# Optimization experiments

Measured on AMD Instinct MI355X. Metric: run time of the kernel, lower is better.

## Reference

```python
import jax, jax.numpy as jnp
import numpy as np

EPS = 1e-6
L, H, D, DFF = 4, 6, 6, 64  # n_layers, num_heads(=dim, head_dim=1), d_hid, ffn hidden


def layernorm(x, w, b):
    mu = jnp.mean(x, axis=-1, keepdims=True)
    var = jnp.mean((x - mu) ** 2, axis=-1, keepdims=True)
    return (x - mu) / jnp.sqrt(var + EPS) * w + b


def autocorr(x, qw, qb, kw, kb, vw, vb, l1w, l1b):
    # x: [B,S,H]; head_dim==1 so per-head Linear is scalar w*x+b per head.
    k_in = jnp.concatenate([x[:, :1], x[:, :-1]], axis=1)   # roll right, first row kept
    v_in = jnp.concatenate([x[:, 1:], x[:, -1:]], axis=1)   # roll left, last row kept
    q = x * qw + qb
    k = k_in * kw + kb
    v = v_in * vw + vb
    teo = q * q - k * v                                      # [B,S,H]
    # nn.LayerNorm([1]) over size-1 axis: mean==x, var==0 -> output is bias
    normed = (teo - teo) / jnp.sqrt(EPS) * l1w + l1b
    scores = jax.nn.softmax(normed, axis=1)                  # over seq dim
    return scores * teo


def mha(x, p, li, ai):
    out = autocorr(x, p['qw'][li, ai], p['qb'][li, ai], p['kw'][li, ai],
                   p['kb'][li, ai], p['vw'][li, ai], p['vb'][li, ai],
                   p['ln1_w'][li, ai], p['ln1_b'][li, ai])
    return layernorm(out + x, p['mha_ln_w'][li, ai], p['mha_ln_b'][li, ai])


def setup_inputs() -> dict:
    key = jax.random.key(0)
    ks = jax.random.split(key, 24)
    n = jax.random.normal
    inp = {
        'x_batch': n(ks[0], (128, 4096, 6), jnp.float32),
        'enc_output': n(ks[1], (128, 4096, 6), jnp.float32),
        'dec_ln_w': jnp.ones((D,), jnp.float32),
        'dec_ln_b': jnp.zeros((D,), jnp.float32),
        'qw': n(ks[2], (L, 2, H), jnp.float32),
        'qb': n(ks[3], (L, 2, H), jnp.float32) * 0.1,
        'kw': n(ks[4], (L, 2, H), jnp.float32),
        'kb': n(ks[5], (L, 2, H), jnp.float32) * 0.1,
        'vw': n(ks[6], (L, 2, H), jnp.float32),
        'vb': n(ks[7], (L, 2, H), jnp.float32) * 0.1,
        'ln1_w': jnp.ones((L, 2), jnp.float32),
        'ln1_b': jnp.zeros((L, 2), jnp.float32),
        'mha_ln_w': jnp.ones((L, 2, D), jnp.float32),
        'mha_ln_b': jnp.zeros((L, 2, D), jnp.float32),
        'ffn_w1': n(ks[8], (L, DFF, D), jnp.float32) * (1.0 / np.sqrt(D)),
        'ffn_b1': jnp.zeros((L, DFF), jnp.float32),
        'ffn_w2': n(ks[9], (L, D, DFF), jnp.float32) * (1.0 / np.sqrt(DFF)),
        'ffn_b2': jnp.zeros((L, D), jnp.float32),
        'ffn_ln_w': jnp.ones((L, D), jnp.float32),
        'ffn_ln_b': jnp.zeros((L, D), jnp.float32),
    }
    return inp


def reference(x_batch, enc_output, dec_ln_w, dec_ln_b, qw, qb, kw, kb, vw, vb,
              ln1_w, ln1_b, mha_ln_w, mha_ln_b, ffn_w1, ffn_b1, ffn_w2, ffn_b2,
              ffn_ln_w, ffn_ln_b):
    p = dict(qw=qw, qb=qb, kw=kw, kb=kb, vw=vw, vb=vb, ln1_w=ln1_w, ln1_b=ln1_b,
             mha_ln_w=mha_ln_w, mha_ln_b=mha_ln_b)
    x = layernorm(x_batch, dec_ln_w, dec_ln_b)  # dropout p=0 -> identity
    for li in range(L):
        x = mha(x, p, li, 0)   # self-attention block
        x = mha(x, p, li, 1)   # "enc" attention block (also self, per source)
        h = jax.nn.relu(jnp.einsum('bsd,fd->bsf', x, ffn_w1[li]) + ffn_b1[li])
        y = jnp.einsum('bsf,df->bsd', h, ffn_w2[li]) + ffn_b2[li] + x
        x = layernorm(y, ffn_ln_w[li], ffn_ln_b[li])
    return x
```

## Files before the change

kernel.cpp:

```cpp
#include <hip/hip_runtime.h>

#define S_LEN  4096
#define DM     6
#define NLAYER 4
#define NFF    64
#define HALO   8
#define TPB    256
#define OUT_PER_WAVE 112
#define BLK_X 10

typedef float    vf2 __attribute__((ext_vector_type(2)));
typedef float    vf4 __attribute__((ext_vector_type(4)));
typedef _Float16 vh4 __attribute__((ext_vector_type(4)));

#define XSZ (128*16)
#define YSTRIDE 130
#define YSZ (6*YSTRIDE*4)
#define WAVE_LDS (XSZ + YSZ)

__device__ __forceinline__ vf2 splat2(float s){ vf2 r; r.x = s; r.y = s; return r; }
__device__ __forceinline__ unsigned pkh(float a, float b){
    return __builtin_bit_cast(unsigned, __builtin_amdgcn_cvt_pkrtz(a, b));
}

__device__ __forceinline__ void ln6v(vf2* v, const float* __restrict__ w,
                                     const float* __restrict__ b) {
    vf2 mu = (((v[0]+v[1])+(v[2]+v[3]))+(v[4]+v[5])) * (1.0f/6.0f);
    vf2 var = splat2(0.0f);
#pragma unroll
    for (int d = 0; d < DM; ++d) { vf2 dd = v[d]-mu; var = __builtin_elementwise_fma(dd, dd, var); }
    vf2 a = var * (1.0f/6.0f) + splat2(1e-6f);
    vf2 r; r.x = rsqrtf(a.x); r.y = rsqrtf(a.y);
#pragma unroll
    for (int d = 0; d < DM; ++d)
        v[d] = __builtin_elementwise_fma((v[d]-mu)*r, splat2(w[d]), splat2(b[d]));
}

__global__ __launch_bounds__(TPB)
void decoder_fused(const float* __restrict__ x_batch,
                   const float* __restrict__ dec_ln_w, const float* __restrict__ dec_ln_b,
                   const float* __restrict__ qw, const float* __restrict__ qb,
                   const float* __restrict__ kw, const float* __restrict__ kb,
                   const float* __restrict__ vw, const float* __restrict__ vb,
                   const float* __restrict__ mha_ln_w, const float* __restrict__ mha_ln_b,
                   const float* __restrict__ ffn_w1, const float* __restrict__ ffn_b1,
                   const float* __restrict__ ffn_w2, const float* __restrict__ ffn_b2,
                   const float* __restrict__ ffn_ln_w, const float* __restrict__ ffn_ln_b,
                   float* __restrict__ out) {
    const int lane = threadIdx.x & 63;
    const int wid  = threadIdx.x >> 6;
    const int w    = blockIdx.x * (TPB/64) + wid;
    const int b    = blockIdx.y;
    const int p    = w * OUT_PER_WAVE - HALO + 2*lane;
    const int c    = lane & 15, g = lane >> 4;

    __shared__ __align__(16) char smem[(TPB/64) * WAVE_LDS];
    char* wbase = smem + wid * WAVE_LDS;
    char* Xb = wbase;
    char* Yb = wbase + XSZ;

    vf2 x2[DM];
    if (p >= 0 && p + 1 < S_LEN) {
        const float4* s = reinterpret_cast<const float4*>(x_batch + ((size_t)b*S_LEN + p)*DM);
        float4 a0 = s[0], a1 = s[1], a2 = s[2];
        x2[0].x=a0.x; x2[1].x=a0.y; x2[2].x=a0.z; x2[3].x=a0.w; x2[4].x=a1.x; x2[5].x=a1.y;
        x2[0].y=a1.z; x2[1].y=a1.w; x2[2].y=a2.x; x2[3].y=a2.y; x2[4].y=a2.z; x2[5].y=a2.w;
    } else {
        const int pc = min(max(p, 0), S_LEN-1);
        const float2* s = reinterpret_cast<const float2*>(x_batch + ((size_t)b*S_LEN + pc)*DM);
        float2 a0 = s[0], a1 = s[1], a2 = s[2];
        x2[0] = splat2(a0.x); x2[1] = splat2(a0.y); x2[2] = splat2(a1.x);
        x2[3] = splat2(a1.y); x2[4] = splat2(a2.x); x2[5] = splat2(a2.y);
    }

    ln6v(x2, dec_ln_w, dec_ln_b);

#pragma unroll 1
    for (int li = 0; li < NLAYER; ++li) {
        vh4 w1f[4], w2f[4]; vf4 b1f[4];
#pragma unroll
        for (int mt = 0; mt < 4; ++mt) {
            const int f = mt*16 + c;
            float4 a = make_float4(0.f, 0.f, 0.f, 0.f);
            if (g == 0) {
                float2 u = *reinterpret_cast<const float2*>(ffn_w1 + li*NFF*DM + f*DM);
                float2 v = *reinterpret_cast<const float2*>(ffn_w1 + li*NFF*DM + f*DM + 2);
                a = make_float4(u.x, u.y, v.x, v.y);
            } else if (g == 1) {
                float2 u = *reinterpret_cast<const float2*>(ffn_w1 + li*NFF*DM + f*DM + 4);
                a = make_float4(u.x, u.y, 0.f, 0.f);
            }
            uint2 ua = make_uint2(pkh(a.x, a.y), pkh(a.z, a.w));
            w1f[mt] = __builtin_bit_cast(vh4, ua);

            float4 wv = make_float4(0.f, 0.f, 0.f, 0.f);
            if (c < DM)
                wv = *reinterpret_cast<const float4*>(ffn_w2 + li*DM*NFF + c*NFF + mt*16 + g*4);
            uint2 uw = make_uint2(pkh(wv.x, wv.y), pkh(wv.z, wv.w));
            w2f[mt] = __builtin_bit_cast(vh4, uw);

            float4 bb = *reinterpret_cast<const float4*>(ffn_b1 + li*NFF + mt*16 + g*4);
            vf4 bv; bv.x=bb.x; bv.y=bb.y; bv.z=bb.z; bv.w=bb.w;
            b1f[mt] = bv;
        }

#pragma unroll 1
        for (int ai = 0; ai < 2; ++ai) {
            const int base = (li*2 + ai) * DM;
            vf2 xm[DM], xp[DM];
#pragma unroll
            for (int d = 0; d < DM; ++d) {
                float up = __shfl_up (x2[d].y, 1);
                float dn = __shfl_down(x2[d].x, 1);
                xm[d].x = (p <= 0) ? x2[d].x : up;
                xm[d].y = x2[d].x;
                xp[d].x = x2[d].y;
                xp[d].y = (p + 1 >= S_LEN - 1) ? x2[d].y : dn;
            }
#pragma unroll
            for (int d = 0; d < DM; ++d) {
                vf2 q = __builtin_elementwise_fma(x2[d], splat2(qw[base+d]), splat2(qb[base+d]));
                vf2 k = __builtin_elementwise_fma(xm[d], splat2(kw[base+d]), splat2(kb[base+d]));
                vf2 v = __builtin_elementwise_fma(xp[d], splat2(vw[base+d]), splat2(vb[base+d]));
                vf2 teo = __builtin_elementwise_fma(q, q, -(k*v));
                x2[d] = __builtin_elementwise_fma(teo, splat2(1.0f/(float)S_LEN), x2[d]);
            }
            ln6v(x2, mha_ln_w + base, mha_ln_b + base);
        }

        {
            {
                char* r0 = Xb + lane*32;
                *(uint4*)r0      = make_uint4(pkh(x2[0].x,x2[1].x), pkh(x2[2].x,x2[3].x),
                                              pkh(x2[4].x,x2[5].x), 0u);
                *(uint4*)(r0+16) = make_uint4(pkh(x2[0].y,x2[1].y), pkh(x2[2].y,x2[3].y),
                                              pkh(x2[4].y,x2[5].y), 0u);
            }
            vh4 bfrag[8];
#pragma unroll
            for (int t = 0; t < 8; ++t) {
                vh4 v = *(const vh4*)(Xb + (16*t + c)*16 + (g&1)*8);
                if (g >= 2) v = (vh4)(_Float16)0;
                bfrag[t] = v;
            }

#pragma unroll
            for (int t = 0; t < 8; ++t) {
                vh4 hb[4];
#pragma unroll
                for (int ft = 0; ft < 4; ++ft) {
                    vf4 hc = __builtin_amdgcn_mfma_f32_16x16x16f16(w1f[ft], bfrag[t], b1f[ft], 0, 0, 0);
                    uint2 u = make_uint2(pkh(hc.x,hc.y), pkh(hc.z,hc.w));
                    vh4 hraw = __builtin_bit_cast(vh4, u);
                    vh4 z4 = (vh4)(_Float16)0;
                    hb[ft] = __builtin_elementwise_max(hraw, z4);
                }
                vf4 yacc; yacc.x=0.f; yacc.y=0.f; yacc.z=0.f; yacc.w=0.f;
#pragma unroll
                for (int ks = 0; ks < 4; ++ks)
                    yacc = __builtin_amdgcn_mfma_f32_16x16x16f16(w2f[ks], hb[ks], yacc, 0, 0, 0);
                int col = 16*t + c;
                float* yp = (float*)Yb;
                if (lane < 32) {
                    yp[(g*4+0)*YSTRIDE + col] = yacc.x;
                    yp[(g*4+1)*YSTRIDE + col] = yacc.y;
                }
                if (lane < 16) {
                    yp[2*YSTRIDE + col] = yacc.z;
                    yp[3*YSTRIDE + col] = yacc.w;
                }
            }
            const float* b2 = ffn_b2 + li*DM;
#pragma unroll
            for (int d = 0; d < DM; ++d) {
                float2 yv = *(const float2*)((float*)Yb + d*YSTRIDE + 2*lane);
                vf2 t2; t2.x = yv.x; t2.y = yv.y;
                x2[d] = x2[d] + splat2(b2[d]) + t2;
            }
            ln6v(x2, ffn_ln_w + li*DM, ffn_ln_b + li*DM);
        }
    }

    if (lane >= 4 && lane < 60 && p < S_LEN) {
        float4* dst = reinterpret_cast<float4*>(out + ((size_t)b*S_LEN + p)*DM);
        float4 a0, a1, a2;
        a0.x=x2[0].x; a0.y=x2[1].x; a0.z=x2[2].x; a0.w=x2[3].x;
        a1.x=x2[4].x; a1.y=x2[5].x; a1.z=x2[0].y; a1.w=x2[1].y;
        a2.x=x2[2].y; a2.y=x2[3].y; a2.z=x2[4].y; a2.w=x2[5].y;
        dst[0]=a0; dst[1]=a1; dst[2]=a2;
    }
}

extern "C" void kernel_launch(void* const* d_in, const int* in_sizes, int n_in,
                              void* d_out, int out_size, void* d_ws, size_t ws_size,
                              hipStream_t stream) {
    const float* x_batch  = (const float*)d_in[0];
    const float* dec_ln_w = (const float*)d_in[2];
    const float* dec_ln_b = (const float*)d_in[3];
    const float* qw       = (const float*)d_in[4];
    const float* qb       = (const float*)d_in[5];
    const float* kw       = (const float*)d_in[6];
    const float* kb       = (const float*)d_in[7];
    const float* vw       = (const float*)d_in[8];
    const float* vb       = (const float*)d_in[9];
    const float* mha_ln_w = (const float*)d_in[12];
    const float* mha_ln_b = (const float*)d_in[13];
    const float* ffn_w1   = (const float*)d_in[14];
    const float* ffn_b1   = (const float*)d_in[15];
    const float* ffn_w2   = (const float*)d_in[16];
    const float* ffn_b2   = (const float*)d_in[17];
    const float* ffn_ln_w = (const float*)d_in[18];
    const float* ffn_ln_b = (const float*)d_in[19];
    float* out = (float*)d_out;

    const int B = in_sizes[0] / (S_LEN * DM);
    dim3 grid(BLK_X, B);
    decoder_fused<<<grid, TPB, 0, stream>>>(
        x_batch, dec_ln_w, dec_ln_b, qw, qb, kw, kb, vw, vb,
        mha_ln_w, mha_ln_b, ffn_w1, ffn_b1, ffn_w2, ffn_b2,
        ffn_ln_w, ffn_ln_b, out);
}
```

Baseline: 140.8 us.

## Process four positions per lane with single-wave blocks and fp16 halo/Y exchange

```diff
diff --git a/kernel.cpp b/kernel.cpp
--- a/kernel.cpp
+++ b/kernel.cpp
@@ -5,35 +5,37 @@
 #define NLAYER 4
 #define NFF    64
 #define HALO   8
-#define TPB    256
-#define OUT_PER_WAVE 112
-#define BLK_X 10
-
-typedef float    vf2 __attribute__((ext_vector_type(2)));
+#define TPB    64
+#define PPL    4
+#define OUT_PER_WAVE 240
+#define WBX    18
+
 typedef float    vf4 __attribute__((ext_vector_type(4)));
+typedef _Float16 vh2 __attribute__((ext_vector_type(2)));
 typedef _Float16 vh4 __attribute__((ext_vector_type(4)));
 
-#define XSZ (128*16)
-#define YSTRIDE 130
-#define YSZ (6*YSTRIDE*4)
-#define WAVE_LDS (XSZ + YSZ)
-
-__device__ __forceinline__ vf2 splat2(float s){ vf2 r; r.x = s; r.y = s; return r; }
+#define XSZ      (256*16)
+#define YSTRIDE  260
+#define YSZ      (3*YSTRIDE*4)
+#define LDS_TOT  (XSZ + YSZ)
+
+__device__ __forceinline__ vf4 splat4(float s){ vf4 r; r.x=s;r.y=s;r.z=s;r.w=s; return r; }
 __device__ __forceinline__ unsigned pkh(float a, float b){
     return __builtin_bit_cast(unsigned, __builtin_amdgcn_cvt_pkrtz(a, b));
 }
-
-__device__ __forceinline__ void ln6v(vf2* v, const float* __restrict__ w,
-                                     const float* __restrict__ b) {
-    vf2 mu = (((v[0]+v[1])+(v[2]+v[3]))+(v[4]+v[5])) * (1.0f/6.0f);
-    vf2 var = splat2(0.0f);
-#pragma unroll
-    for (int d = 0; d < DM; ++d) { vf2 dd = v[d]-mu; var = __builtin_elementwise_fma(dd, dd, var); }
-    vf2 a = var * (1.0f/6.0f) + splat2(1e-6f);
-    vf2 r; r.x = rsqrtf(a.x); r.y = rsqrtf(a.y);
+__device__ __forceinline__ vh2 bch2(unsigned u){ return __builtin_bit_cast(vh2, u); }
+
+__device__ __forceinline__ void ln6v4(vf4* v, const float* __restrict__ w,
+                                      const float* __restrict__ b) {
+    vf4 mu = (((v[0]+v[1])+(v[2]+v[3]))+(v[4]+v[5])) * (1.0f/6.0f);
+    vf4 var = splat4(0.0f);
+#pragma unroll
+    for (int d = 0; d < DM; ++d) { vf4 dd = v[d]-mu; var = __builtin_elementwise_fma(dd, dd, var); }
+    vf4 a = var * (1.0f/6.0f) + splat4(1e-6f);
+    vf4 r; r.x=rsqrtf(a.x); r.y=rsqrtf(a.y); r.z=rsqrtf(a.z); r.w=rsqrtf(a.w);
 #pragma unroll
     for (int d = 0; d < DM; ++d)
-        v[d] = __builtin_elementwise_fma((v[d]-mu)*r, splat2(w[d]), splat2(b[d]));
+        v[d] = __builtin_elementwise_fma((v[d]-mu)*r, splat4(w[d]), splat4(b[d]));
 }
 
 __global__ __launch_bounds__(TPB)
@@ -47,33 +49,42 @@
                    const float* __restrict__ ffn_w2, const float* __restrict__ ffn_b2,
                    const float* __restrict__ ffn_ln_w, const float* __restrict__ ffn_ln_b,
                    float* __restrict__ out) {
-    const int lane = threadIdx.x & 63;
-    const int wid  = threadIdx.x >> 6;
-    const int w    = blockIdx.x * (TPB/64) + wid;
+    const int lane = threadIdx.x;
+    const int w    = blockIdx.x;
     const int b    = blockIdx.y;
-    const int p    = w * OUT_PER_WAVE - HALO + 2*lane;
+    const int p0   = w * OUT_PER_WAVE - HALO + PPL*lane;
     const int c    = lane & 15, g = lane >> 4;
 
-    __shared__ __align__(16) char smem[(TPB/64) * WAVE_LDS];
-    char* wbase = smem + wid * WAVE_LDS;
-    char* Xb = wbase;
-    char* Yb = wbase + XSZ;
-
-    vf2 x2[DM];
-    if (p >= 0 && p + 1 < S_LEN) {
-        const float4* s = reinterpret_cast<const float4*>(x_batch + ((size_t)b*S_LEN + p)*DM);
-        float4 a0 = s[0], a1 = s[1], a2 = s[2];
-        x2[0].x=a0.x; x2[1].x=a0.y; x2[2].x=a0.z; x2[3].x=a0.w; x2[4].x=a1.x; x2[5].x=a1.y;
-        x2[0].y=a1.z; x2[1].y=a1.w; x2[2].y=a2.x; x2[3].y=a2.y; x2[4].y=a2.z; x2[5].y=a2.w;
+    __shared__ __align__(16) char smem[LDS_TOT];
+    char* Xb = smem;
+    char* Yb = smem + XSZ;
+
+    vf4 x4[DM];
+    if (p0 >= 0 && p0 + PPL <= S_LEN) {
+        const float4* s = reinterpret_cast<const float4*>(x_batch + ((size_t)b*S_LEN + p0)*DM);
+        float4 a0=s[0],a1=s[1],a2=s[2],a3=s[3],a4=s[4],a5=s[5];
+        x4[0] = (vf4){a0.x, a1.z, a3.x, a4.z};
+        x4[1] = (vf4){a0.y, a1.w, a3.y, a4.w};
+        x4[2] = (vf4){a0.z, a2.x, a3.z, a5.x};
+        x4[3] = (vf4){a0.w, a2.y, a3.w, a5.y};
+        x4[4] = (vf4){a1.x, a2.z, a4.x, a5.z};
+        x4[5] = (vf4){a1.y, a2.w, a4.y, a5.w};
     } else {
-        const int pc = min(max(p, 0), S_LEN-1);
-        const float2* s = reinterpret_cast<const float2*>(x_batch + ((size_t)b*S_LEN + pc)*DM);
-        float2 a0 = s[0], a1 = s[1], a2 = s[2];
-        x2[0] = splat2(a0.x); x2[1] = splat2(a0.y); x2[2] = splat2(a1.x);
-        x2[3] = splat2(a1.y); x2[4] = splat2(a2.x); x2[5] = splat2(a2.y);
+        float tmp[PPL][DM];
+#pragma unroll
+        for (int s = 0; s < PPL; ++s) {
+            const int pc = min(max(p0 + s, 0), S_LEN-1);
+            const float2* f2 = reinterpret_cast<const float2*>(x_batch + ((size_t)b*S_LEN + pc)*DM);
+            float2 u0 = f2[0], u1 = f2[1], u2 = f2[2];
+            tmp[s][0]=u0.x; tmp[s][1]=u0.y; tmp[s][2]=u1.x;
+            tmp[s][3]=u1.y; tmp[s][4]=u2.x; tmp[s][5]=u2.y;
+        }
+#pragma unroll
+        for (int d = 0; d < DM; ++d)
+            x4[d] = (vf4){tmp[0][d], tmp[1][d], tmp[2][d], tmp[3][d]};
     }
 
-    ln6v(x2, dec_ln_w, dec_ln_b);
+    ln6v4(x4, dec_ln_w, dec_ln_b);
 
 #pragma unroll 1
     for (int li = 0; li < NLAYER; ++li) {
@@ -100,94 +111,99 @@
             w2f[mt] = __builtin_bit_cast(vh4, uw);
 
             float4 bb = *reinterpret_cast<const float4*>(ffn_b1 + li*NFF + mt*16 + g*4);
-            vf4 bv; bv.x=bb.x; bv.y=bb.y; bv.z=bb.z; bv.w=bb.w;
-            b1f[mt] = bv;
+            b1f[mt] = (vf4){bb.x, bb.y, bb.z, bb.w};
         }
 
 #pragma unroll 1
         for (int ai = 0; ai < 2; ++ai) {
             const int base = (li*2 + ai) * DM;
-            vf2 xm[DM], xp[DM];
+            unsigned s3a = pkh(x4[0].w, x4[1].w), s3b = pkh(x4[2].w, x4[3].w), s3c = pkh(x4[4].w, x4[5].w);
+            unsigned s0a = pkh(x4[0].x, x4[1].x), s0b = pkh(x4[2].x, x4[3].x), s0c = pkh(x4[4].x, x4[5].x);
+            unsigned ua = __shfl_up((int)s3a, 1), ub = __shfl_up((int)s3b, 1), uc = __shfl_up((int)s3c, 1);
+            unsigned da = __shfl_down((int)s0a, 1), db = __shfl_down((int)s0b, 1), dc = __shfl_down((int)s0c, 1);
+            float pm[DM], pp[DM];
+            { vh2 h; h=bch2(ua); pm[0]=(float)h.x; pm[1]=(float)h.y;
+                     h=bch2(ub); pm[2]=(float)h.x; pm[3]=(float)h.y;
+                     h=bch2(uc); pm[4]=(float)h.x; pm[5]=(float)h.y;
+                     h=bch2(da); pp[0]=(float)h.x; pp[1]=(float)h.y;
+                     h=bch2(db); pp[2]=(float)h.x; pp[3]=(float)h.y;
+                     h=bch2(dc); pp[4]=(float)h.x; pp[5]=(float)h.y; }
+            const bool first = (p0 <= 0);
+            const bool last  = (p0 + PPL - 1 >= S_LEN - 1);
 #pragma unroll
             for (int d = 0; d < DM; ++d) {
-                float up = __shfl_up (x2[d].y, 1);
-                float dn = __shfl_down(x2[d].x, 1);
-                xm[d].x = (p <= 0) ? x2[d].x : up;
-                xm[d].y = x2[d].x;
-                xp[d].x = x2[d].y;
-                xp[d].y = (p + 1 >= S_LEN - 1) ? x2[d].y : dn;
-            }
-#pragma unroll
-            for (int d = 0; d < DM; ++d) {
-                vf2 q = __builtin_elementwise_fma(x2[d], splat2(qw[base+d]), splat2(qb[base+d]));
-                vf2 k = __builtin_elementwise_fma(xm[d], splat2(kw[base+d]), splat2(kb[base+d]));
-                vf2 v = __builtin_elementwise_fma(xp[d], splat2(vw[base+d]), splat2(vb[base+d]));
-                vf2 teo = __builtin_elementwise_fma(q, q, -(k*v));
-                x2[d] = __builtin_elementwise_fma(teo, splat2(1.0f/(float)S_LEN), x2[d]);
-            }
-            ln6v(x2, mha_ln_w + base, mha_ln_b + base);
+                float prevv = first ? x4[d].x : pm[d];
+                float nextv = last  ? x4[d].w : pp[d];
+                vf4 xm = (vf4){prevv,   x4[d].x, x4[d].y, x4[d].z};
+                vf4 xp = (vf4){x4[d].y, x4[d].z, x4[d].w, nextv};
+                vf4 q = __builtin_elementwise_fma(x4[d], splat4(qw[base+d]), splat4(qb[base+d]));
+                vf4 k = __builtin_elementwise_fma(xm,    splat4(kw[base+d]), splat4(kb[base+d]));
+                vf4 v = __builtin_elementwise_fma(xp,    splat4(vw[base+d]), splat4(vb[base+d]));
+                vf4 teo = __builtin_elementwise_fma(q, q, -(k*v));
+                x4[d] = __builtin_elementwise_fma(teo, splat4(1.0f/(float)S_LEN), x4[d]);
+            }
+            ln6v4(x4, mha_ln_w + base, mha_ln_b + base);
         }
 
         {
             {
-                char* r0 = Xb + lane*32;
-                *(uint4*)r0      = make_uint4(pkh(x2[0].x,x2[1].x), pkh(x2[2].x,x2[3].x),
-                                              pkh(x2[4].x,x2[5].x), 0u);
-                *(uint4*)(r0+16) = make_uint4(pkh(x2[0].y,x2[1].y), pkh(x2[2].y,x2[3].y),
-                                              pkh(x2[4].y,x2[5].y), 0u);
-            }
-            vh4 bfrag[8];
-#pragma unroll
-            for (int t = 0; t < 8; ++t) {
+                char* r0 = Xb + lane*64;
+                *(uint4*)(r0)    = make_uint4(pkh(x4[0].x,x4[1].x), pkh(x4[2].x,x4[3].x), pkh(x4[4].x,x4[5].x), 0u);
+                *(uint4*)(r0+16) = make_uint4(pkh(x4[0].y,x4[1].y), pkh(x4[2].y,x4[3].y), pkh(x4[4].y,x4[5].y), 0u);
+                *(uint4*)(r0+32) = make_uint4(pkh(x4[0].z,x4[1].z), pkh(x4[2].z,x4[3].z), pkh(x4[4].z,x4[5].z), 0u);
+                *(uint4*)(r0+48) = make_uint4(pkh(x4[0].w,x4[1].w), pkh(x4[2].w,x4[3].w), pkh(x4[4].w,x4[5].w), 0u);
+            }
+            vh4 bfrag[16];
+#pragma unroll
+            for (int t = 0; t < 16; ++t) {
                 vh4 v = *(const vh4*)(Xb + (16*t + c)*16 + (g&1)*8);
                 if (g >= 2) v = (vh4)(_Float16)0;
                 bfrag[t] = v;
             }
 
 #pragma unroll
-            for (int t = 0; t < 8; ++t) {
+            for (int t = 0; t < 16; ++t) {
                 vh4 hb[4];
 #pragma unroll
                 for (int ft = 0; ft < 4; ++ft) {
                     vf4 hc = __builtin_amdgcn_mfma_f32_16x16x16f16(w1f[ft], bfrag[t], b1f[ft], 0, 0, 0);
                     uint2 u = make_uint2(pkh(hc.x,hc.y), pkh(hc.z,hc.w));
                     vh4 hraw = __builtin_bit_cast(vh4, u);
-                    vh4 z4 = (vh4)(_Float16)0;
-                    hb[ft] = __builtin_elementwise_max(hraw, z4);
+                    hb[ft] = __builtin_elementwise_max(hraw, (vh4)(_Float16)0);
                 }
                 vf4 yacc; yacc.x=0.f; yacc.y=0.f; yacc.z=0.f; yacc.w=0.f;
 #pragma unroll
                 for (int ks = 0; ks < 4; ++ks)
                     yacc = __builtin_amdgcn_mfma_f32_16x16x16f16(w2f[ks], hb[ks], yacc, 0, 0, 0);
-                int col = 16*t + c;
-                float* yp = (float*)Yb;
-                if (lane < 32) {
-                    yp[(g*4+0)*YSTRIDE + col] = yacc.x;
-                    yp[(g*4+1)*YSTRIDE + col] = yacc.y;
-                }
-                if (lane < 16) {
-                    yp[2*YSTRIDE + col] = yacc.z;
-                    yp[3*YSTRIDE + col] = yacc.w;
-                }
+                const int col = 16*t + c;
+                unsigned* yp = (unsigned*)Yb;
+                if (lane < 32)
+                    yp[(g*2)*YSTRIDE + col] = pkh(yacc.x, yacc.y);
+                if (lane < 16)
+                    yp[1*YSTRIDE + col] = pkh(yacc.z, yacc.w);
             }
             const float* b2 = ffn_b2 + li*DM;
 #pragma unroll
-            for (int d = 0; d < DM; ++d) {
-                float2 yv = *(const float2*)((float*)Yb + d*YSTRIDE + 2*lane);
-                vf2 t2; t2.x = yv.x; t2.y = yv.y;
-                x2[d] = x2[d] + splat2(b2[d]) + t2;
-            }
-            ln6v(x2, ffn_ln_w + li*DM, ffn_ln_b + li*DM);
+            for (int pr = 0; pr < 3; ++pr) {
+                uint4 u = *(const uint4*)((unsigned*)Yb + pr*YSTRIDE + 4*lane);
+                vh2 h0 = bch2(u.x), h1 = bch2(u.y), h2 = bch2(u.z), h3 = bch2(u.w);
+                vf4 ylo = (vf4){(float)h0.x, (float)h1.x, (float)h2.x, (float)h3.x};
+                vf4 yhi = (vf4){(float)h0.y, (float)h1.y, (float)h2.y, (float)h3.y};
+                x4[2*pr]   = x4[2*pr]   + splat4(b2[2*pr])   + ylo;
+                x4[2*pr+1] = x4[2*pr+1] + splat4(b2[2*pr+1]) + yhi;
+            }
+            ln6v4(x4, ffn_ln_w + li*DM, ffn_ln_b + li*DM);
         }
     }
 
-    if (lane >= 4 && lane < 60 && p < S_LEN) {
-        float4* dst = reinterpret_cast<float4*>(out + ((size_t)b*S_LEN + p)*DM);
-        float4 a0, a1, a2;
-        a0.x=x2[0].x; a0.y=x2[1].x; a0.z=x2[2].x; a0.w=x2[3].x;
-        a1.x=x2[4].x; a1.y=x2[5].x; a1.z=x2[0].y; a1.w=x2[1].y;
-        a2.x=x2[2].y; a2.y=x2[3].y; a2.z=x2[4].y; a2.w=x2[5].y;
-        dst[0]=a0; dst[1]=a1; dst[2]=a2;
+    if (lane >= 2 && lane < 62 && p0 < S_LEN) {
+        float4* dst = reinterpret_cast<float4*>(out + ((size_t)b*S_LEN + p0)*DM);
+        dst[0] = make_float4(x4[0].x, x4[1].x, x4[2].x, x4[3].x);
+        dst[1] = make_float4(x4[4].x, x4[5].x, x4[0].y, x4[1].y);
+        dst[2] = make_float4(x4[2].y, x4[3].y, x4[4].y, x4[5].y);
+        dst[3] = make_float4(x4[0].z, x4[1].z, x4[2].z, x4[3].z);
+        dst[4] = make_float4(x4[4].z, x4[5].z, x4[0].w, x4[1].w);
+        dst[5] = make_float4(x4[2].w, x4[3].w, x4[4].w, x4[5].w);
     }
 }
 
@@ -214,7 +230,7 @@
     float* out = (float*)d_out;
 
     const int B = in_sizes[0] / (S_LEN * DM);
-    dim3 grid(BLK_X, B);
+    dim3 grid(WBX, B);
     decoder_fused<<<grid, TPB, 0, stream>>>(
         x_batch, dec_ln_w, dec_ln_b, qw, qb, kw, kb, vw, vb,
         mha_ln_w, mha_ln_b, ffn_w1, ffn_b1, ffn_w2, ffn_b2,
```

After: 145.6 us. 3.4% more time.
